# Kernel tuning notes

Hardware: AMD Instinct MI355X
Metric: run time of the kernel (lower is better)

The kernel has to match this reference:

```python
import jax, jax.numpy as jnp
import numpy as np


def setup_inputs() -> dict:
    key = jax.random.key(0)
    k1, k2, k3, k4 = jax.random.split(key, 4)
    B, N, D, L = 4, 512, 256, 64
    x = jax.random.normal(k1, (B, N, D), dtype=jnp.float32)
    adj = jax.random.uniform(k2, (B, N, N), dtype=jnp.float32)
    W_proj = jax.random.normal(k3, (L, D), dtype=jnp.float32) * (1.0 / np.sqrt(D))
    learn_w = jax.random.uniform(k4, (L,), dtype=jnp.float32)  # init.uniform_(0,1)
    return {"x": x, "adj": adj, "W_proj": W_proj, "learn_w": learn_w}


def reference(x, adj, W_proj, learn_w):
    # x: [B,N,D]; projection (no bias): x_hat [B,N,L]
    x_hat = jnp.einsum('bnd,ld->bnl', x, W_proj)
    # pairwise L1-style abs difference: [B,N,N,L]
    diff = jnp.abs(x_hat[:, :, None, :] - x_hat[:, None, :, :])
    # weighted reduce over feature dim: [B,N,N]
    dist = jnp.einsum('bijl,l->bij', diff, learn_w)
    out = jax.nn.leaky_relu(dist, negative_slope=0.01)
    out = out - jnp.max(out, axis=-1, keepdims=True)
    soft_adj = adj * jnp.exp(out)
    # NOTE: faithful to original: epsilon added AFTER the division
    soft_adj = soft_adj / jnp.sum(soft_adj, axis=-1, keepdims=True) + 1e-10
    return soft_adj
```

## Files before the change

### kernel.cpp

```cpp
#include <hip/hip_runtime.h>
#include <math.h>

#define BB 4
#define NN 512
#define DD 256
#define LL 64

#define WST 260
#define IPB 4

__global__ __launch_bounds__(512) void k1_proj(const float* __restrict__ x,
                                               const float* __restrict__ Wp,
                                               const float* __restrict__ lw,
                                               float* __restrict__ xhatT) {
  __shared__ __align__(16) float Wl[LL * WST];
  __shared__ __align__(16) float xs[8 * WST];
  const int bx = blockIdx.x;
  const int b  = bx >> 6;
  const int n0 = (bx & 63) * 8;
  const int t  = threadIdx.x;

  const float4* Wp4 = (const float4*)Wp;
  #pragma unroll
  for (int it = 0; it < 8; ++it) {
    int idx = it * 512 + t;
    int ll  = idx >> 6;
    int dq  = idx & 63;
    *(float4*)&Wl[ll * WST + dq * 4] = Wp4[idx];
  }
  {
    const float4* x4 = (const float4*)(x + ((size_t)b * NN + n0) * DD);
    *(float4*)&xs[(t >> 6) * WST + (t & 63) * 4] = x4[t];
  }
  __syncthreads();

  const int l = t >> 3;
  const int r = t & 7;
  const float4* wrow = (const float4*)&Wl[l * WST];
  const float4* xrow = (const float4*)&xs[r * WST];
  float4 a = make_float4(0.f, 0.f, 0.f, 0.f);
  #pragma unroll 8
  for (int dd = 0; dd < 64; ++dd) {
    float4 wv = wrow[dd];
    float4 xv = xrow[dd];
    a.x += xv.x * wv.x;
    a.y += xv.y * wv.y;
    a.z += xv.z * wv.z;
    a.w += xv.w * wv.w;
  }
  xhatT[((size_t)b * LL + l) * NN + n0 + r] =
      lw[l] * ((a.x + a.y) + (a.z + a.w));
}

__global__ __launch_bounds__(512, 4) void k2_main(const float* __restrict__ xhatT,
                                                  const float* __restrict__ adj,
                                                  float* __restrict__ out) {
  __shared__ float redm[IPB * 8];
  __shared__ float reds[IPB * 8];

  const int bx   = blockIdx.x;
  const int b    = bx >> 7;
  const int i0   = (bx & 127) * IPB;
  const int t    = threadIdx.x;
  const int wave = t >> 6;
  const int lane = t & 63;

  const float* xb = xhatT + (size_t)b * (LL * NN);

  const float* adjb = adj + ((size_t)b * NN + i0) * NN;
  float adjv[IPB];
  #pragma unroll
  for (int r = 0; r < IPB; ++r) adjv[r] = adjb[(size_t)r * NN + t];

  float acc[IPB] = {0.f, 0.f, 0.f, 0.f};
  #pragma unroll 8
  for (int l = 0; l < LL; ++l) {
    float  p  = xb[l * NN + t];
    float4 xi = *(const float4*)(xb + l * NN + i0);
    acc[0] += fabsf(xi.x - p);
    acc[1] += fabsf(xi.y - p);
    acc[2] += fabsf(xi.z - p);
    acc[3] += fabsf(xi.w - p);
  }

  #pragma unroll
  for (int r = 0; r < IPB; ++r) {
    float d = acc[r];
    acc[r] = d >= 0.f ? d : 0.01f * d;
  }

  #pragma unroll
  for (int r = 0; r < IPB; ++r) {
    float m = acc[r];
    #pragma unroll
    for (int off = 32; off > 0; off >>= 1)
      m = fmaxf(m, __shfl_xor(m, off, 64));
    if (lane == 0) redm[r * 8 + wave] = m;
  }
  __syncthreads();

  float e[IPB];
  #pragma unroll
  for (int r = 0; r < IPB; ++r) {
    float m = redm[r * 8 + 0];
    #pragma unroll
    for (int k = 1; k < 8; ++k) m = fmaxf(m, redm[r * 8 + k]);
    e[r] = adjv[r] * __expf(acc[r] - m);
  }

  #pragma unroll
  for (int r = 0; r < IPB; ++r) {
    float s = e[r];
    #pragma unroll
    for (int off = 32; off > 0; off >>= 1)
      s += __shfl_xor(s, off, 64);
    if (lane == 0) reds[r * 8 + wave] = s;
  }
  __syncthreads();

  float* outb = out + ((size_t)b * NN + i0) * NN;
  #pragma unroll
  for (int r = 0; r < IPB; ++r) {
    float s = reds[r * 8 + 0];
    #pragma unroll
    for (int k = 1; k < 8; ++k) s += reds[r * 8 + k];
    outb[(size_t)r * NN + t] = e[r] / s + 1e-10f;
  }
}

extern "C" void kernel_launch(void* const* d_in, const int* in_sizes, int n_in,
                              void* d_out, int out_size, void* d_ws, size_t ws_size,
                              hipStream_t stream) {
  const float* x   = (const float*)d_in[0];
  const float* adj = (const float*)d_in[1];
  const float* Wp  = (const float*)d_in[2];
  const float* lw  = (const float*)d_in[3];
  float* out   = (float*)d_out;
  float* xhatT = (float*)d_ws;

  hipLaunchKernelGGL(k1_proj, dim3(BB * NN / 8), dim3(512), 0, stream,
                     x, Wp, lw, xhatT);
  hipLaunchKernelGGL(k2_main, dim3(BB * NN / IPB), dim3(512), 0, stream,
                     xhatT, adj, out);
}
```

Measured before the change: 74.93 us.

## Store xhat row-major and stage query rows in shared memory for pairwise L1

The projection kernel now writes xhat as [B,N,L] instead of transposed [B,L,N], and remaps its thread-to-(l,r) mapping so the stores stay somewhat grouped. The main kernel stages the four query rows in shared memory, and each thread reads its own xhat row with float4 loads in place of strided scalar loads per feature. In exchange, each thread's row loads are now strided by 256 bytes across lanes, which gives uncoalesced access patterns. A shared-memory stage and an extra barrier are also added.

```diff
diff --git a/kernel.cpp b/kernel.cpp
--- a/kernel.cpp
+++ b/kernel.cpp
@@ -12,13 +12,15 @@
 __global__ __launch_bounds__(512) void k1_proj(const float* __restrict__ x,
                                                const float* __restrict__ Wp,
                                                const float* __restrict__ lw,
-                                               float* __restrict__ xhatT) {
+                                               float* __restrict__ xhat) {
   __shared__ __align__(16) float Wl[LL * WST];
   __shared__ __align__(16) float xs[8 * WST];
-  const int bx = blockIdx.x;
-  const int b  = bx >> 6;
-  const int n0 = (bx & 63) * 8;
-  const int t  = threadIdx.x;
+  const int bx   = blockIdx.x;
+  const int b    = bx >> 6;
+  const int n0   = (bx & 63) * 8;
+  const int t    = threadIdx.x;
+  const int wave = t >> 6;
+  const int lane = t & 63;
 
   const float4* Wp4 = (const float4*)Wp;
   #pragma unroll
@@ -30,12 +32,12 @@
   }
   {
     const float4* x4 = (const float4*)(x + ((size_t)b * NN + n0) * DD);
-    *(float4*)&xs[(t >> 6) * WST + (t & 63) * 4] = x4[t];
+    *(float4*)&xs[wave * WST + lane * 4] = x4[t];
   }
   __syncthreads();
 
-  const int l = t >> 3;
-  const int r = t & 7;
+  const int l = (wave << 3) | (t & 7);
+  const int r = (t >> 3) & 7;
   const float4* wrow = (const float4*)&Wl[l * WST];
   const float4* xrow = (const float4*)&xs[r * WST];
   float4 a = make_float4(0.f, 0.f, 0.f, 0.f);
@@ -48,13 +50,14 @@
     a.z += xv.z * wv.z;
     a.w += xv.w * wv.w;
   }
-  xhatT[((size_t)b * LL + l) * NN + n0 + r] =
+  xhat[((size_t)b * NN + n0 + r) * LL + l] =
       lw[l] * ((a.x + a.y) + (a.z + a.w));
 }
 
-__global__ __launch_bounds__(512, 4) void k2_main(const float* __restrict__ xhatT,
+__global__ __launch_bounds__(512, 4) void k2_main(const float* __restrict__ xhat,
                                                   const float* __restrict__ adj,
                                                   float* __restrict__ out) {
+  __shared__ __align__(16) float4 xi4[IPB * 16];
   __shared__ float redm[IPB * 8];
   __shared__ float reds[IPB * 8];
 
@@ -65,22 +68,28 @@
   const int wave = t >> 6;
   const int lane = t & 63;
 
-  const float* xb = xhatT + (size_t)b * (LL * NN);
+  const float* xbase = xhat + (size_t)b * NN * LL;
 
   const float* adjb = adj + ((size_t)b * NN + i0) * NN;
   float adjv[IPB];
   #pragma unroll
   for (int r = 0; r < IPB; ++r) adjv[r] = adjb[(size_t)r * NN + t];
 
+  if (t < IPB * 16)
+    xi4[t] = ((const float4*)(xbase + (size_t)(i0 + (t >> 4)) * LL))[t & 15];
+  __syncthreads();
+
+  const float4* xr = (const float4*)(xbase + (size_t)t * LL);
   float acc[IPB] = {0.f, 0.f, 0.f, 0.f};
-  #pragma unroll 8
-  for (int l = 0; l < LL; ++l) {
-    float  p  = xb[l * NN + t];
-    float4 xi = *(const float4*)(xb + l * NN + i0);
-    acc[0] += fabsf(xi.x - p);
-    acc[1] += fabsf(xi.y - p);
-    acc[2] += fabsf(xi.z - p);
-    acc[3] += fabsf(xi.w - p);
+  #pragma unroll
+  for (int c = 0; c < 16; ++c) {
+    float4 xj = xr[c];
+    #pragma unroll
+    for (int r = 0; r < IPB; ++r) {
+      float4 xi = xi4[r * 16 + c];
+      acc[r] += fabsf(xi.x - xj.x) + fabsf(xi.y - xj.y) +
+                fabsf(xi.z - xj.z) + fabsf(xi.w - xj.w);
+    }
   }
 
   #pragma unroll
@@ -135,11 +144,11 @@
   const float* adj = (const float*)d_in[1];
   const float* Wp  = (const float*)d_in[2];
   const float* lw  = (const float*)d_in[3];
-  float* out   = (float*)d_out;
-  float* xhatT = (float*)d_ws;
+  float* out  = (float*)d_out;
+  float* xhat = (float*)d_ws;
 
   hipLaunchKernelGGL(k1_proj, dim3(BB * NN / 8), dim3(512), 0, stream,
-                     x, Wp, lw, xhatT);
+                     x, Wp, lw, xhat);
   hipLaunchKernelGGL(k2_main, dim3(BB * NN / IPB), dim3(512), 0, stream,
-                     xhatT, adj, out);
+                     xhat, adj, out);
 }
```

Measured after the change: 126.6 us. +69.0%, slower.
